# Kernel optimization log

Measured on AMD Instinct MI355X. Metric: run time of the kernel, lower is better.

## Reference

```python
import jax, jax.numpy as jnp
import numpy as np

D_MODEL = 1024
N_HEAD = 16
D_HEAD = D_MODEL // N_HEAD


def setup_inputs() -> dict:
    key = jax.random.key(0)
    ks = jax.random.split(key, 5)
    x = jax.random.normal(ks[0], (4, 2048, D_MODEL), dtype=jnp.float32)
    s = 1.0 / np.sqrt(D_MODEL)
    W_qkv = jax.random.normal(ks[1], (D_MODEL, 3 * D_MODEL), dtype=jnp.float32) * s
    b_qkv = jnp.zeros((3 * D_MODEL,), dtype=jnp.float32)
    W_out = jax.random.normal(ks[2], (D_MODEL, D_MODEL), dtype=jnp.float32) * s
    b_out = jnp.zeros((D_MODEL,), dtype=jnp.float32)
    return {"x": x, "W_qkv": W_qkv, "b_qkv": b_qkv, "W_out": W_out, "b_out": b_out}


def reference(x, W_qkv, b_qkv, W_out, b_out):
    B, T, C = x.shape
    qkv = x @ W_qkv + b_qkv                      # [B,T,3C]
    q, k, v = jnp.split(qkv, 3, axis=-1)
    def heads(t):
        return t.reshape(B, T, N_HEAD, D_HEAD).transpose(0, 2, 1, 3)  # [B,H,T,Dh]
    q, k, v = heads(q), heads(k), heads(v)
    scale = 1.0 / np.sqrt(D_HEAD)
    attn = jnp.einsum('bhqd,bhkd->bhqk', q, k) * scale  # [B,H,T,T]
    causal = jnp.tril(jnp.ones((T, T), dtype=bool))
    attn = jnp.where(causal, attn, -jnp.inf)
    attn = jax.nn.softmax(attn, axis=-1)
    out = jnp.einsum('bhqk,bhkd->bhqd', attn, v)  # [B,H,T,Dh]
    out = out.transpose(0, 2, 1, 3).reshape(B, T, C)
    return out @ W_out + b_out
```

## Files before the change

### kernel.cpp

```cpp
#include <hip/hip_runtime.h>

typedef __bf16 bf16;
typedef __bf16 bf16x4 __attribute__((ext_vector_type(4)));
typedef __bf16 bf16x8 __attribute__((ext_vector_type(8)));
typedef float f32x4 __attribute__((ext_vector_type(4)));

#define AS1C(p) ((const __attribute__((address_space(1))) void*)(p))
#define AS3(p)  ((__attribute__((address_space(3))) void*)(p))

#define T_SEQ 2048
#define QK_LD 2048

__global__ void cvt_f32_bf16(const float* __restrict__ X, bf16* __restrict__ Y, int n) {
    int i = (blockIdx.x * 256 + threadIdx.x) * 4;
    if (i >= n) return;
    const float4 f = *(const float4*)(X + i);
    bf16x4 o;
    o.x = (bf16)f.x; o.y = (bf16)f.y; o.z = (bf16)f.z; o.w = (bf16)f.w;
    *(bf16x4*)(Y + i) = o;
}

__global__ void transpose_cvt(const float* __restrict__ W, bf16* __restrict__ Wt,
                              int R, int C) {
    __shared__ float tile[32][33];
    const int bx = blockIdx.x * 32;
    const int by = blockIdx.y * 32;
    const int tx = threadIdx.x, ty = threadIdx.y;
#pragma unroll
    for (int i = 0; i < 32; i += 8)
        tile[ty + i][tx] = W[(size_t)(by + ty + i) * C + bx + tx];
    __syncthreads();
#pragma unroll
    for (int i = 0; i < 32; i += 8)
        Wt[(size_t)(bx + ty + i) * R + by + tx] = (bf16)tile[tx][ty + i];
}

template <bool OUT_BF16, bool SPLIT_V>
__global__ __launch_bounds__(256, 2)
void gemm_bt(const bf16* __restrict__ A, const bf16* __restrict__ Bt,
             const float* __restrict__ bias, void* __restrict__ Cout,
             bf16* __restrict__ Vtb, int M, int N, int K, int ldC) {
    __shared__ bf16 sm[2 * 16384 / 2];

    const int t = threadIdx.x;
    const int lane = t & 63, quad = lane >> 4, l16 = lane & 15;
    const int wave = t >> 6;
    const int wm = (wave >> 1) * 64;
    const int wn = (wave & 1) * 64;
    const long m0 = (long)blockIdx.y * 128;
    const long n0 = (long)blockIdx.x * 128;

    f32x4 acc[4][4] = {};

    const int srow = t >> 2;
    const int skb  = (t & 3) ^ ((srow >> 1) & 3);
    const bf16* aptr0 = A  + (m0 + srow) * (long)K + skb * 8;
    const bf16* aptr1 = aptr0 + (long)64 * K;
    const bf16* bptr0 = Bt + (n0 + srow) * (long)K + skb * 8;
    const bf16* bptr1 = bptr0 + (long)64 * K;

    int offA[4], offB[4];
#pragma unroll
    for (int i = 0; i < 4; ++i) {
        const int row = wm + i * 16 + l16;
        offA[i] = (row * 4 + (quad ^ ((row >> 1) & 3))) * 8;
    }
#pragma unroll
    for (int j = 0; j < 4; ++j) {
        const int row = wn + j * 16 + l16;
        offB[j] = 4096 + (row * 4 + (quad ^ ((row >> 1) & 3))) * 8;
    }

    auto stage = [&](int buf, int k0) {
        bf16* base = &sm[buf * 8192];
        __builtin_amdgcn_global_load_lds(AS1C(aptr0 + k0), AS3(base + t * 8),        16, 0, 0);
        __builtin_amdgcn_global_load_lds(AS1C(aptr1 + k0), AS3(base + 2048 + t * 8), 16, 0, 0);
        __builtin_amdgcn_global_load_lds(AS1C(bptr0 + k0), AS3(base + 4096 + t * 8), 16, 0, 0);
        __builtin_amdgcn_global_load_lds(AS1C(bptr1 + k0), AS3(base + 6144 + t * 8), 16, 0, 0);
    };
    auto compute = [&](int buf) {
        const bf16* s = &sm[buf * 8192];
        bf16x8 af[4], bfr[4];
#pragma unroll
        for (int i = 0; i < 4; ++i) af[i] = *(const bf16x8*)(s + offA[i]);
#pragma unroll
        for (int j = 0; j < 4; ++j) bfr[j] = *(const bf16x8*)(s + offB[j]);
#pragma unroll
        for (int i = 0; i < 4; ++i)
#pragma unroll
            for (int j = 0; j < 4; ++j)
                acc[i][j] = __builtin_amdgcn_mfma_f32_16x16x32_bf16(bfr[j], af[i], acc[i][j], 0, 0, 0);
    };

    stage(0, 0);
    for (int k0 = 0; k0 < K; k0 += 64) {
        __syncthreads();
        if (k0 + 32 < K) stage(1, k0 + 32);
        compute(0);
        __syncthreads();
        if (k0 + 64 < K) stage(0, k0 + 64);
        compute(1);
    }

    bf16*  Cb = (bf16*)Cout;
    float* Cf = (float*)Cout;
    const bool vblock = SPLIT_V && (n0 >= 2048);
#pragma unroll
    for (int i = 0; i < 4; ++i) {
        const long gm = m0 + wm + i * 16 + l16;
#pragma unroll
        for (int j = 0; j < 4; ++j) {
            const int nloc = wn + j * 16 + quad * 4;
            const long n = n0 + nloc;
            const float4 bv = *(const float4*)(bias + n);
            float v[4];
#pragma unroll
            for (int r = 0; r < 4; ++r) v[r] = acc[i][j][r] + (&bv.x)[r];
            if (vblock) {
                const int bb = (int)(gm >> 11), tok = (int)(gm & 2047);
                const int nv = (int)(n - 2048);
                const int h = nv >> 6, d0 = nv & 63;
                bf16* dst = Vtb + ((size_t)(bb * 16 + h) * 64 + d0) * T_SEQ + tok;
#pragma unroll
                for (int r = 0; r < 4; ++r) dst[(size_t)r * T_SEQ] = (bf16)v[r];
            } else if (OUT_BF16) {
                bf16x4 o;
#pragma unroll
                for (int r = 0; r < 4; ++r) o[r] = (bf16)v[r];
                *(bf16x4*)(Cb + gm * ldC + n) = o;
            } else {
                float4 o;
#pragma unroll
                for (int r = 0; r < 4; ++r) (&o.x)[r] = v[r];
                *(float4*)(Cf + gm * ldC + n) = o;
            }
        }
    }
}

__global__ __launch_bounds__(256, 2)
void attn_kernel(const bf16* __restrict__ qk, const bf16* __restrict__ vtb,
                 bf16* __restrict__ Out) {
    const int bh = blockIdx.x;
    const int qt = 15 - (int)blockIdx.y;
    const int b = bh >> 4, h = bh & 15;
    const int t = threadIdx.x;
    const int wave = t >> 6, lane = t & 63, quad = lane >> 4, l16 = lane & 15;
    const int wq = wave * 32;
    const int q0 = qt * 128;

    __shared__ bf16 Ks[4096];
    __shared__ bf16 VTs[4096];
    __shared__ bf16 Ps[128][72];

    const bf16* Qg = qk + (size_t)b * T_SEQ * QK_LD + h * 64;
    const bf16* Kg = Qg + 1024;
    const bf16* vth = vtb + (size_t)bh * 64 * T_SEQ;

    for (int c = t; c < 1024; c += 256) {
        const int row = c >> 3, col8 = (c & 7) * 8;
        *(uint4*)&Ps[row][col8] = *(const uint4*)(Qg + (size_t)(q0 + row) * QK_LD + col8);
    }
    __syncthreads();
    const float qsc = 0.125f * 1.4426950408889634f;
    bf16x8 qf[2][2];
#pragma unroll
    for (int jt = 0; jt < 2; ++jt)
#pragma unroll
        for (int s = 0; s < 2; ++s) {
            bf16x8 v = *(const bf16x8*)&Ps[wq + jt * 16 + l16][s * 32 + quad * 8];
#pragma unroll
            for (int e = 0; e < 8; ++e) v[e] = (bf16)((float)v[e] * qsc);
            qf[jt][s] = v;
        }

    const int sr = t >> 3;
    const int skb = (t & 7) ^ (sr & 7);
    const bf16* kp0 = Kg + (size_t)sr * QK_LD + skb * 8;
    const bf16* kp1 = kp0 + (size_t)32 * QK_LD;
    const bf16* vp0 = vth + (size_t)sr * T_SEQ + skb * 8;
    const bf16* vp1 = vp0 + (size_t)32 * T_SEQ;

    int offK[4][2], offV[4][2];
#pragma unroll
    for (int it = 0; it < 4; ++it) {
        const int row = it * 16 + l16;
#pragma unroll
        for (int s = 0; s < 2; ++s) {
            const int kb = s * 4 + quad;
            offK[it][s] = (row * 8 + (kb ^ (row & 7))) * 8;
            offV[it][s] = offK[it][s];
        }
    }

    f32x4 oacc[4][2] = {};
    float lsum[2] = {0.f, 0.f};
    const int nkt = qt * 2 + 2;

    uint4 kr0, kr1, vr0, vr1;
    kr0 = *(const uint4*)kp0;  kr1 = *(const uint4*)kp1;
    vr0 = *(const uint4*)vp0;  vr1 = *(const uint4*)vp1;

    for (int kt = 0; kt < nkt; ++kt) {
        const int k0 = kt * 64;
        __syncthreads();
        *(uint4*)(Ks  + t * 8)        = kr0;
        *(uint4*)(Ks  + 2048 + t * 8) = kr1;
        *(uint4*)(VTs + t * 8)        = vr0;
        *(uint4*)(VTs + 2048 + t * 8) = vr1;
        __syncthreads();

        if (kt + 1 < nkt) {
            const int kn = k0 + 64;
            kr0 = *(const uint4*)(kp0 + (size_t)kn * QK_LD);
            kr1 = *(const uint4*)(kp1 + (size_t)kn * QK_LD);
            vr0 = *(const uint4*)(vp0 + kn);
            vr1 = *(const uint4*)(vp1 + kn);
        }

        f32x4 sacc[4][2] = {};
#pragma unroll
        for (int s = 0; s < 2; ++s) {
            bf16x8 kf[4];
#pragma unroll
            for (int it = 0; it < 4; ++it)
                kf[it] = *(const bf16x8*)(Ks + offK[it][s]);
#pragma unroll
            for (int it = 0; it < 4; ++it)
#pragma unroll
                for (int jt = 0; jt < 2; ++jt)
                    sacc[it][jt] = __builtin_amdgcn_mfma_f32_16x16x32_bf16(kf[it], qf[jt][s], sacc[it][jt], 0, 0, 0);
        }

        const bool need_mask = (kt >= 2 * qt);
#pragma unroll
        for (int it = 0; it < 4; ++it)
#pragma unroll
            for (int jt = 0; jt < 2; ++jt) {
                bf16x4 pb;
                if (need_mask) {
                    const int qrow = q0 + wq + jt * 16 + l16;
                    const int kbase = k0 + it * 16 + quad * 4;
#pragma unroll
                    for (int r = 0; r < 4; ++r) {
                        float p = (kbase + r > qrow) ? 0.f : exp2f(sacc[it][jt][r]);
                        lsum[jt] += p;
                        pb[r] = (bf16)p;
                    }
                } else {
#pragma unroll
                    for (int r = 0; r < 4; ++r) {
                        const float p = exp2f(sacc[it][jt][r]);
                        lsum[jt] += p;
                        pb[r] = (bf16)p;
                    }
                }
                *(bf16x4*)&Ps[wq + jt * 16 + l16][it * 16 + quad * 4] = pb;
            }

#pragma unroll
        for (int s2 = 0; s2 < 2; ++s2) {
            bf16x8 vf[4], pf[2];
#pragma unroll
            for (int it2 = 0; it2 < 4; ++it2)
                vf[it2] = *(const bf16x8*)(VTs + offV[it2][s2]);
#pragma unroll
            for (int jt = 0; jt < 2; ++jt)
                pf[jt] = *(const bf16x8*)&Ps[wq + jt * 16 + l16][s2 * 32 + quad * 8];
#pragma unroll
            for (int it2 = 0; it2 < 4; ++it2)
#pragma unroll
                for (int jt = 0; jt < 2; ++jt)
                    oacc[it2][jt] = __builtin_amdgcn_mfma_f32_16x16x32_bf16(vf[it2], pf[jt], oacc[it2][jt], 0, 0, 0);
        }
    }

    float inv[2];
#pragma unroll
    for (int jt = 0; jt < 2; ++jt) {
        float l = lsum[jt];
        l += __shfl_xor(l, 16);
        l += __shfl_xor(l, 32);
        inv[jt] = 1.0f / l;
    }
#pragma unroll
    for (int it2 = 0; it2 < 4; ++it2)
#pragma unroll
        for (int jt = 0; jt < 2; ++jt) {
            bf16x4 ob;
#pragma unroll
            for (int r = 0; r < 4; ++r) ob[r] = (bf16)(oacc[it2][jt][r] * inv[jt]);
            const int qrow = q0 + wq + jt * 16 + l16;
            const int dcol = h * 64 + it2 * 16 + quad * 4;
            *(bf16x4*)&Out[(size_t)(b * T_SEQ + qrow) * 1024 + dcol] = ob;
        }
}

extern "C" void kernel_launch(void* const* d_in, const int* in_sizes, int n_in,
                              void* d_out, int out_size, void* d_ws, size_t ws_size,
                              hipStream_t stream) {
    const float* x     = (const float*)d_in[0];
    const float* W_qkv = (const float*)d_in[1];
    const float* b_qkv = (const float*)d_in[2];
    const float* W_out = (const float*)d_in[3];
    const float* b_out = (const float*)d_in[4];
    float* out = (float*)d_out;

    char* ws = (char*)d_ws;
    bf16* xb   = (bf16*)ws; ws += (size_t)8192 * 1024 * 2;
    bf16* wtq  = (bf16*)ws; ws += (size_t)3072 * 1024 * 2;
    bf16* wto  = (bf16*)ws; ws += (size_t)1024 * 1024 * 2;
    bf16* qkb  = (bf16*)ws; ws += (size_t)8192 * 2048 * 2;
    bf16* vtb  = (bf16*)ws; ws += (size_t)64 * 64 * 2048 * 2;
    bf16* aout = (bf16*)ws; ws += (size_t)8192 * 1024 * 2;

    cvt_f32_bf16<<<8192, 256, 0, stream>>>(x, xb, 8192 * 1024);
    transpose_cvt<<<dim3(96, 32), dim3(32, 8), 0, stream>>>(W_qkv, wtq, 1024, 3072);
    transpose_cvt<<<dim3(32, 32), dim3(32, 8), 0, stream>>>(W_out, wto, 1024, 1024);

    gemm_bt<true, true><<<dim3(24, 64), 256, 0, stream>>>(
        xb, wtq, b_qkv, (void*)qkb, vtb, 8192, 3072, 1024, 2048);
    attn_kernel<<<dim3(64, 16), 256, 0, stream>>>(qkb, vtb, aout);
    gemm_bt<false, false><<<dim3(8, 64), 256, 0, stream>>>(
        aout, wto, b_out, (void*)out, nullptr, 8192, 1024, 1024, 1024);
}
```

Measured before the change: 261.4 us.

## Double-buffer K/V tiles, swizzle P tile, use native exp2, raise occupancy

The attention kernel now double-buffers the K and V shared-memory tiles, which drops the leading barrier in each key-tile iteration. The P/Q staging tile is replaced with an unpadded XOR-swizzled layout, and exp2f is swapped for the native exp2 intrinsic. Launch bounds are raised on both the GEMM and attention kernels to allow more resident blocks, and the GEMM shared array declaration is changed to an equivalent size. The trade-offs are possible register pressure from the higher occupancy targets and slightly lower exp precision.

```diff
diff --git a/kernel.cpp b/kernel.cpp
--- a/kernel.cpp
+++ b/kernel.cpp
@@ -10,6 +10,8 @@
 
 #define T_SEQ 2048
 #define QK_LD 2048
+
+extern "C" __device__ float __ocml_native_exp2_f32(float);
 
 __global__ void cvt_f32_bf16(const float* __restrict__ X, bf16* __restrict__ Y, int n) {
     int i = (blockIdx.x * 256 + threadIdx.x) * 4;
@@ -36,11 +38,11 @@
 }
 
 template <bool OUT_BF16, bool SPLIT_V>
-__global__ __launch_bounds__(256, 2)
+__global__ __launch_bounds__(256, 4)
 void gemm_bt(const bf16* __restrict__ A, const bf16* __restrict__ Bt,
              const float* __restrict__ bias, void* __restrict__ Cout,
              bf16* __restrict__ Vtb, int M, int N, int K, int ldC) {
-    __shared__ bf16 sm[2 * 16384 / 2];
+    __shared__ bf16 sm[16384];
 
     const int t = threadIdx.x;
     const int lane = t & 63, quad = lane >> 4, l16 = lane & 15;
@@ -138,7 +140,7 @@
     }
 }
 
-__global__ __launch_bounds__(256, 2)
+__global__ __launch_bounds__(256, 3)
 void attn_kernel(const bf16* __restrict__ qk, const bf16* __restrict__ vtb,
                  bf16* __restrict__ Out) {
     const int bh = blockIdx.x;
@@ -149,17 +151,18 @@
     const int wq = wave * 32;
     const int q0 = qt * 128;
 
-    __shared__ bf16 Ks[4096];
-    __shared__ bf16 VTs[4096];
-    __shared__ bf16 Ps[128][72];
+    __shared__ bf16 Ks[2][4096];
+    __shared__ bf16 VTs[2][4096];
+    __shared__ bf16 Ps[8192];
 
     const bf16* Qg = qk + (size_t)b * T_SEQ * QK_LD + h * 64;
     const bf16* Kg = Qg + 1024;
     const bf16* vth = vtb + (size_t)bh * 64 * T_SEQ;
 
     for (int c = t; c < 1024; c += 256) {
-        const int row = c >> 3, col8 = (c & 7) * 8;
-        *(uint4*)&Ps[row][col8] = *(const uint4*)(Qg + (size_t)(q0 + row) * QK_LD + col8);
+        const int row = c >> 3, kb = c & 7;
+        *(uint4*)(Ps + row * 64 + (((kb ^ (row & 7)) << 3))) =
+            *(const uint4*)(Qg + (size_t)(q0 + row) * QK_LD + kb * 8);
     }
     __syncthreads();
     const float qsc = 0.125f * 1.4426950408889634f;
@@ -168,7 +171,8 @@
     for (int jt = 0; jt < 2; ++jt)
 #pragma unroll
         for (int s = 0; s < 2; ++s) {
-            bf16x8 v = *(const bf16x8*)&Ps[wq + jt * 16 + l16][s * 32 + quad * 8];
+            const int row = wq + jt * 16 + l16;
+            bf16x8 v = *(const bf16x8*)(Ps + row * 64 + (((s * 4 + quad) ^ (row & 7)) << 3));
 #pragma unroll
             for (int e = 0; e < 8; ++e) v[e] = (bf16)((float)v[e] * qsc);
             qf[jt][s] = v;
@@ -181,33 +185,30 @@
     const bf16* vp0 = vth + (size_t)sr * T_SEQ + skb * 8;
     const bf16* vp1 = vp0 + (size_t)32 * T_SEQ;
 
-    int offK[4][2], offV[4][2];
-#pragma unroll
-    for (int it = 0; it < 4; ++it) {
-        const int row = it * 16 + l16;
+    int offKV[4][2];
+#pragma unroll
+    for (int it = 0; it < 4; ++it)
 #pragma unroll
         for (int s = 0; s < 2; ++s) {
-            const int kb = s * 4 + quad;
-            offK[it][s] = (row * 8 + (kb ^ (row & 7))) * 8;
-            offV[it][s] = offK[it][s];
-        }
-    }
+            const int row = it * 16 + l16;
+            offKV[it][s] = row * 64 + (((s * 4 + quad) ^ (row & 7)) << 3);
+        }
 
     f32x4 oacc[4][2] = {};
     float lsum[2] = {0.f, 0.f};
     const int nkt = qt * 2 + 2;
 
-    uint4 kr0, kr1, vr0, vr1;
-    kr0 = *(const uint4*)kp0;  kr1 = *(const uint4*)kp1;
-    vr0 = *(const uint4*)vp0;  vr1 = *(const uint4*)vp1;
+    uint4 kr0 = *(const uint4*)kp0, kr1 = *(const uint4*)kp1;
+    uint4 vr0 = *(const uint4*)vp0, vr1 = *(const uint4*)vp1;
 
     for (int kt = 0; kt < nkt; ++kt) {
         const int k0 = kt * 64;
-        __syncthreads();
-        *(uint4*)(Ks  + t * 8)        = kr0;
-        *(uint4*)(Ks  + 2048 + t * 8) = kr1;
-        *(uint4*)(VTs + t * 8)        = vr0;
-        *(uint4*)(VTs + 2048 + t * 8) = vr1;
+        bf16* kb_ = Ks[kt & 1];
+        bf16* vb_ = VTs[kt & 1];
+        *(uint4*)(kb_ + t * 8)        = kr0;
+        *(uint4*)(kb_ + 2048 + t * 8) = kr1;
+        *(uint4*)(vb_ + t * 8)        = vr0;
+        *(uint4*)(vb_ + 2048 + t * 8) = vr1;
         __syncthreads();
 
         if (kt + 1 < nkt) {
@@ -224,7 +225,7 @@
             bf16x8 kf[4];
 #pragma unroll
             for (int it = 0; it < 4; ++it)
-                kf[it] = *(const bf16x8*)(Ks + offK[it][s]);
+                kf[it] = *(const bf16x8*)(kb_ + offKV[it][s]);
 #pragma unroll
             for (int it = 0; it < 4; ++it)
 #pragma unroll
@@ -237,25 +238,28 @@
         for (int it = 0; it < 4; ++it)
 #pragma unroll
             for (int jt = 0; jt < 2; ++jt) {
+                const int prow = wq + jt * 16 + l16;
                 bf16x4 pb;
                 if (need_mask) {
-                    const int qrow = q0 + wq + jt * 16 + l16;
+                    const int qrow = q0 + prow;
                     const int kbase = k0 + it * 16 + quad * 4;
 #pragma unroll
                     for (int r = 0; r < 4; ++r) {
-                        float p = (kbase + r > qrow) ? 0.f : exp2f(sacc[it][jt][r]);
+                        const float e = __ocml_native_exp2_f32(sacc[it][jt][r]);
+                        const float p = (kbase + r > qrow) ? 0.f : e;
                         lsum[jt] += p;
                         pb[r] = (bf16)p;
                     }
                 } else {
 #pragma unroll
                     for (int r = 0; r < 4; ++r) {
-                        const float p = exp2f(sacc[it][jt][r]);
+                        const float p = __ocml_native_exp2_f32(sacc[it][jt][r]);
                         lsum[jt] += p;
                         pb[r] = (bf16)p;
                     }
                 }
-                *(bf16x4*)&Ps[wq + jt * 16 + l16][it * 16 + quad * 4] = pb;
+                *(bf16x4*)(Ps + prow * 64 +
+                           (((it * 2 + (quad >> 1)) ^ (prow & 7)) << 3) + ((quad & 1) << 2)) = pb;
             }
 
 #pragma unroll
@@ -263,10 +267,12 @@
             bf16x8 vf[4], pf[2];
 #pragma unroll
             for (int it2 = 0; it2 < 4; ++it2)
-                vf[it2] = *(const bf16x8*)(VTs + offV[it2][s2]);
-#pragma unroll
-            for (int jt = 0; jt < 2; ++jt)
-                pf[jt] = *(const bf16x8*)&Ps[wq + jt * 16 + l16][s2 * 32 + quad * 8];
+                vf[it2] = *(const bf16x8*)(vb_ + offKV[it2][s2]);
+#pragma unroll
+            for (int jt = 0; jt < 2; ++jt) {
+                const int prow = wq + jt * 16 + l16;
+                pf[jt] = *(const bf16x8*)(Ps + prow * 64 + (((s2 * 4 + quad) ^ (prow & 7)) << 3));
+            }
 #pragma unroll
             for (int it2 = 0; it2 < 4; ++it2)
 #pragma unroll
```

New measurement: 246.1 us. 1.06x faster.
